# Performance work log

Measured on AMD Instinct MI355X. Metric: run time of the kernel, lower is better.

Reference implementation:

```python
import jax, jax.numpy as jnp
import numpy as np

N = 100000      # num_nodes
E = 1600000     # num_edges
F_IN = 5        # in_features
H = 64          # hidden_channels
HC = H // 2     # classifier hidden
L = 3           # num GCN layers
EPS = 1e-5      # BatchNorm eps


def setup_inputs() -> dict:
    key = jax.random.key(0)
    ks = jax.random.split(key, 12)
    s = 0.1
    return {
        "x": jax.random.normal(ks[0], (N, F_IN), dtype=jnp.float32),
        "edge_index": jax.random.randint(ks[1], (2, E), 0, N, dtype=jnp.int32),
        "W_in": jax.random.normal(ks[2], (F_IN, H), dtype=jnp.float32) * s,
        "b_in": jax.random.normal(ks[3], (H,), dtype=jnp.float32) * s,
        "conv_W": jax.random.normal(ks[4], (L, H, H), dtype=jnp.float32) * s,
        "conv_b": jax.random.normal(ks[5], (L, H), dtype=jnp.float32) * s,
        "bn_gamma": jnp.ones((L, H), dtype=jnp.float32),
        "bn_beta": jnp.zeros((L, H), dtype=jnp.float32),
        "W1": jax.random.normal(ks[6], (H, HC), dtype=jnp.float32) * s,
        "b1": jax.random.normal(ks[7], (HC,), dtype=jnp.float32) * s,
        "W2": jax.random.normal(ks[8], (HC, 1), dtype=jnp.float32) * s,
        "b2": jax.random.normal(ks[9], (1,), dtype=jnp.float32) * s,
    }


def reference(x, edge_index, W_in, b_in, conv_W, conv_b, bn_gamma, bn_beta, W1, b1, W2, b2):
    src, dst = edge_index[0], edge_index[1]

    # input projection + ReLU
    h = jax.nn.relu(x @ W_in + b_in)  # (N, H)

    # GCN symmetric normalization with self-loops (PyG GCNConv default):
    # deg includes the self-loop weight of 1.
    deg = jax.ops.segment_sum(jnp.ones((E,), dtype=h.dtype), dst, num_segments=N) + 1.0
    dinv = jax.lax.rsqrt(deg)                       # deg^{-1/2}, (N,)
    edge_coef = dinv[src] * dinv[dst]               # (E,)
    self_coef = dinv * dinv                         # (N,)

    for i in range(L):
        hw = h @ conv_W[i]                          # linear (no bias yet), (N, H)
        # gather -> scale -> scatter-add aggregation, plus self-loop term
        agg = jax.ops.segment_sum(hw[src] * edge_coef[:, None], dst, num_segments=N)
        agg = agg + hw * self_coef[:, None] + conv_b[i]
        # BatchNorm1d over nodes (batch statistics; eval dropout = identity)
        mean = jnp.mean(agg, axis=0)
        var = jnp.var(agg, axis=0)
        h = bn_gamma[i] * (agg - mean) * jax.lax.rsqrt(var + EPS) + bn_beta[i]
        h = jax.nn.relu(h)

    # classifier MLP: H -> H//2 -> 1, squeeze to (N,)
    logits = (jax.nn.relu(h @ W1 + b1) @ W2 + b2).squeeze(-1)
    return logits
```

## Files before the change

### kernel.cpp

```cpp
#include <hip/hip_runtime.h>

#define NN 100000
#define EE 1600000
#define EPSV 1e-5f
#define QW 12500

using short8 = __attribute__((ext_vector_type(8))) short;
using floatx4 = __attribute__((ext_vector_type(4))) float;

__device__ __forceinline__ unsigned short f2bf(float f) {
    union { float f; unsigned int u; } cv;
    cv.f = f;
    unsigned int u = cv.u;
    u += 0x7FFFu + ((u >> 16) & 1u);
    return (unsigned short)(u >> 16);
}

__device__ __forceinline__ float bf2f(unsigned short u) {
    union { unsigned int i; float f; } cv;
    cv.i = ((unsigned int)u) << 16;
    return cv.f;
}

__global__ void deg_kernel(const int* __restrict__ dst, int* __restrict__ degi8) {
    int e = blockIdx.x * 256 + threadIdx.x;
    if (e >= EE) return;
    int q = blockIdx.x & 7;
    atomicAdd(&degi8[q * NN + dst[e]], 1);
}

__global__ void scan1(const int* __restrict__ degi8, int* __restrict__ degi,
                      int* __restrict__ offsets, int* __restrict__ partial,
                      float* __restrict__ dinv) {
    __shared__ int sdata[256];
    int t = threadIdx.x;
    int n = blockIdx.x * 256 + t;
    int v = 0;
    if (n < NN) {
#pragma unroll
        for (int q = 0; q < 8; ++q) v += degi8[q * NN + n];
        degi[n] = v;
        dinv[n] = rsqrtf((float)v + 1.0f);
    }
    sdata[t] = v;
    __syncthreads();
    for (int off = 1; off < 256; off <<= 1) {
        int x = (t >= off) ? sdata[t - off] : 0;
        __syncthreads();
        sdata[t] += x;
        __syncthreads();
    }
    if (n < NN) offsets[n] = sdata[t] - v;
    if (t == 255) partial[blockIdx.x] = sdata[255];
}

__global__ void scan2(int* __restrict__ partial, int* __restrict__ partial_pref,
                      int nparts, float* __restrict__ stats) {
    __shared__ int sdata[512];
    int t = threadIdx.x;
    if (t < 384) stats[t] = 0.f;
    int v = (t < nparts) ? partial[t] : 0;
    sdata[t] = v;
    __syncthreads();
    for (int off = 1; off < 512; off <<= 1) {
        int x = (t >= off) ? sdata[t - off] : 0;
        __syncthreads();
        sdata[t] += x;
        __syncthreads();
    }
    if (t < nparts) partial_pref[t] = sdata[t] - v;
}

__global__ void fill_kernel(const int* __restrict__ src, const int* __restrict__ dst,
                            int* __restrict__ offsets,
                            const int* __restrict__ partial_pref,
                            const float* __restrict__ dinv,
                            int2* __restrict__ sorted) {
    int q = blockIdx.x & 7;
    int e = (blockIdx.x >> 3) * 256 + threadIdx.x;
    if (e >= EE) return;
    int d = dst[e];
    if ((unsigned)(d - q * QW) >= (unsigned)QW) return;
    int s = src[e];
    int idx = partial_pref[d >> 8] + atomicAdd(&offsets[d], 1);
    int2 rec;
    rec.x = s;
    rec.y = __float_as_int(dinv[s] * dinv[d]);
    sorted[idx] = rec;
}

__global__ __launch_bounds__(256) void gemm64_bn(const float* __restrict__ in,
                                                 const float* __restrict__ x,
                                                 const float* __restrict__ Win,
                                                 const float* __restrict__ bin,
                                                 const float* __restrict__ stats,
                                                 const float* __restrict__ gamma,
                                                 const float* __restrict__ beta,
                                                 const float* __restrict__ W,
                                                 unsigned short* __restrict__ out,
                                                 int mode) {
    __shared__ __align__(16) unsigned short As[64 * 72];
    __shared__ __align__(16) unsigned short Wt[64 * 72];
    __shared__ float scale[64], shift[64];
    __shared__ float Wins[320];
    __shared__ float bins[64];
    int t = threadIdx.x;
    if (mode == 1) {
        if (t < 64) {
            const float invN = 1.0f / (float)NN;
            float mean = stats[t] * invN;
            float var = stats[64 + t] * invN - mean * mean;
            float rstd = rsqrtf(var + EPSV);
            float sc = gamma[t] * rstd;
            scale[t] = sc;
            shift[t] = beta[t] - mean * sc;
        }
    } else {
        for (int i = t; i < 320; i += 256) Wins[i] = Win[i];
        if (t < 64) bins[t] = bin[t];
    }
    for (int i = t; i < 4096; i += 256) {
        int k = i >> 6, c = i & 63;
        Wt[c * 72 + k] = f2bf(W[k * 64 + c]);
    }
    __syncthreads();
    int base = blockIdx.x * 64;
    if (mode == 1) {
        for (int i = t; i < 4096; i += 256) {
            int r = i >> 6, c = i & 63;
            float v = 0.f;
            if (base + r < NN) {
                v = in[(base + r) * 64 + c];
                v = fmaxf(v * scale[c] + shift[c], 0.f);
            }
            As[r * 72 + c] = f2bf(v);
        }
    } else {
        for (int i = t; i < 4096; i += 256) {
            int r = i >> 6, c = i & 63;
            int n = base + r;
            float v = 0.f;
            if (n < NN) {
                float acc = bins[c];
#pragma unroll
                for (int k = 0; k < 5; ++k) acc += x[n * 5 + k] * Wins[k * 64 + c];
                v = fmaxf(acc, 0.f);
            }
            As[r * 72 + c] = f2bf(v);
        }
    }
    __syncthreads();
    int wv = t >> 6;
    int lane = t & 63;
    int quad = lane >> 4;
    int mm = lane & 15;
    short8 a0 = *(const short8*)&As[(wv * 16 + mm) * 72 + quad * 8];
    short8 a1 = *(const short8*)&As[(wv * 16 + mm) * 72 + 32 + quad * 8];
#pragma unroll
    for (int ct = 0; ct < 4; ++ct) {
        short8 b0 = *(const short8*)&Wt[(ct * 16 + mm) * 72 + quad * 8];
        short8 b1 = *(const short8*)&Wt[(ct * 16 + mm) * 72 + 32 + quad * 8];
        floatx4 acc = {0.f, 0.f, 0.f, 0.f};
        acc = __builtin_amdgcn_mfma_f32_16x16x32_bf16(a0, b0, acc, 0, 0, 0);
        acc = __builtin_amdgcn_mfma_f32_16x16x32_bf16(a1, b1, acc, 0, 0, 0);
#pragma unroll
        for (int reg = 0; reg < 4; ++reg) {
            int n = base + wv * 16 + quad * 4 + reg;
            if (n < NN) out[n * 64 + ct * 16 + mm] = f2bf(acc[reg]);
        }
    }
}

__global__ __launch_bounds__(256) void agg_kernel(const unsigned int* __restrict__ hw32,
                                                  const int2* __restrict__ sorted,
                                                  const int* __restrict__ offsets,
                                                  const int* __restrict__ partial_pref,
                                                  const int* __restrict__ degi,
                                                  const float* __restrict__ dinv,
                                                  const float* __restrict__ b,
                                                  float* __restrict__ agg,
                                                  float* __restrict__ stats) {
    int t = threadIdx.x;
    int lane = t & 63;
    int w = t >> 6;
    int half = lane >> 5;
    int c2 = lane & 31;
    float b0 = b[2 * c2], b1v = b[2 * c2 + 1];
    float bsx = 0.f, bsy = 0.f, bqx = 0.f, bqy = 0.f;
    for (int n = blockIdx.x * 4 + w; n < NN; n += gridDim.x * 4) {
        int cnt = degi[n];
        int start = partial_pref[n >> 8] + offsets[n] - cnt;
        float di = dinv[n];
        float ax = 0.f, ay = 0.f;
        if (half == 0) {
            unsigned int u = hw32[n * 32 + c2];
            float sc = di * di;
            ax = bf2f((unsigned short)(u & 0xffffu)) * sc + b0;
            ay = bf2f((unsigned short)(u >> 16)) * sc + b1v;
        }
        for (int base = 0; base < cnt; base += 64) {
            int m = min(64, cnt - base);
            int2 rec = make_int2(0, 0);
            if (lane < m) rec = sorted[start + base + lane];
            int k = 0;
            for (; k + 16 <= m; k += 16) {
                int e0 = k + half, e1 = k + 2 + half, e2 = k + 4 + half, e3 = k + 6 + half;
                int e4 = k + 8 + half, e5 = k + 10 + half, e6 = k + 12 + half, e7 = k + 14 + half;
                int s0 = __shfl(rec.x, e0), s1 = __shfl(rec.x, e1);
                int s2 = __shfl(rec.x, e2), s3 = __shfl(rec.x, e3);
                int s4 = __shfl(rec.x, e4), s5 = __shfl(rec.x, e5);
                int s6 = __shfl(rec.x, e6), s7 = __shfl(rec.x, e7);
                unsigned int u0 = hw32[s0 * 32 + c2];
                unsigned int u1 = hw32[s1 * 32 + c2];
                unsigned int u2 = hw32[s2 * 32 + c2];
                unsigned int u3 = hw32[s3 * 32 + c2];
                unsigned int u4 = hw32[s4 * 32 + c2];
                unsigned int u5 = hw32[s5 * 32 + c2];
                unsigned int u6 = hw32[s6 * 32 + c2];
                unsigned int u7 = hw32[s7 * 32 + c2];
                float c0 = __int_as_float(__shfl(rec.y, e0));
                float c1 = __int_as_float(__shfl(rec.y, e1));
                float c2f = __int_as_float(__shfl(rec.y, e2));
                float c3 = __int_as_float(__shfl(rec.y, e3));
                float c4 = __int_as_float(__shfl(rec.y, e4));
                float c5 = __int_as_float(__shfl(rec.y, e5));
                float c6 = __int_as_float(__shfl(rec.y, e6));
                float c7 = __int_as_float(__shfl(rec.y, e7));
                ax += bf2f((unsigned short)(u0 & 0xffffu)) * c0;
                ay += bf2f((unsigned short)(u0 >> 16)) * c0;
                ax += bf2f((unsigned short)(u1 & 0xffffu)) * c1;
                ay += bf2f((unsigned short)(u1 >> 16)) * c1;
                ax += bf2f((unsigned short)(u2 & 0xffffu)) * c2f;
                ay += bf2f((unsigned short)(u2 >> 16)) * c2f;
                ax += bf2f((unsigned short)(u3 & 0xffffu)) * c3;
                ay += bf2f((unsigned short)(u3 >> 16)) * c3;
                ax += bf2f((unsigned short)(u4 & 0xffffu)) * c4;
                ay += bf2f((unsigned short)(u4 >> 16)) * c4;
                ax += bf2f((unsigned short)(u5 & 0xffffu)) * c5;
                ay += bf2f((unsigned short)(u5 >> 16)) * c5;
                ax += bf2f((unsigned short)(u6 & 0xffffu)) * c6;
                ay += bf2f((unsigned short)(u6 >> 16)) * c6;
                ax += bf2f((unsigned short)(u7 & 0xffffu)) * c7;
                ay += bf2f((unsigned short)(u7 >> 16)) * c7;
            }
            for (; k + 4 <= m; k += 4) {
                int e0 = k + half, e1 = k + 2 + half;
                int s0 = __shfl(rec.x, e0), s1 = __shfl(rec.x, e1);
                unsigned int u0 = hw32[s0 * 32 + c2];
                unsigned int u1 = hw32[s1 * 32 + c2];
                float c0 = __int_as_float(__shfl(rec.y, e0));
                float c1 = __int_as_float(__shfl(rec.y, e1));
                ax += bf2f((unsigned short)(u0 & 0xffffu)) * c0;
                ay += bf2f((unsigned short)(u0 >> 16)) * c0;
                ax += bf2f((unsigned short)(u1 & 0xffffu)) * c1;
                ay += bf2f((unsigned short)(u1 >> 16)) * c1;
            }
            for (; k < m; k += 2) {
                int e = k + half;
                int s = __shfl(rec.x, e);
                float cf = __int_as_float(__shfl(rec.y, e));
                unsigned int u = hw32[s * 32 + c2];
                ax += bf2f((unsigned short)(u & 0xffffu)) * cf;
                ay += bf2f((unsigned short)(u >> 16)) * cf;
            }
        }
        ax += __shfl_xor(ax, 32);
        ay += __shfl_xor(ay, 32);
        if (half == 0) {
            float2 v = make_float2(ax, ay);
            *(float2*)&agg[n * 64 + 2 * c2] = v;
            bsx += ax;
            bsy += ay;
            bqx += ax * ax;
            bqy += ay * ay;
        }
    }
    __shared__ float red[2][4][64];
    if (half == 0) {
        red[0][w][2 * c2] = bsx;
        red[0][w][2 * c2 + 1] = bsy;
        red[1][w][2 * c2] = bqx;
        red[1][w][2 * c2 + 1] = bqy;
    }
    __syncthreads();
    if (w == 0) {
        int c = t;
        float s = red[0][0][c] + red[0][1][c] + red[0][2][c] + red[0][3][c];
        float ss = red[1][0][c] + red[1][1][c] + red[1][2][c] + red[1][3][c];
        atomicAdd(&stats[c], s);
        atomicAdd(&stats[64 + c], ss);
    }
}

__global__ __launch_bounds__(256) void classifier(const float* __restrict__ agg,
                                                  const float* __restrict__ stats,
                                                  const float* __restrict__ gamma,
                                                  const float* __restrict__ beta,
                                                  const float* __restrict__ W1,
                                                  const float* __restrict__ b1,
                                                  const float* __restrict__ W2,
                                                  const float* __restrict__ b2,
                                                  float* __restrict__ out) {
    __shared__ float W1s[2048];
    __shared__ float b1s[32];
    __shared__ float W2s[32];
    __shared__ float scale[64], shift[64];
    int t = threadIdx.x;
    for (int i = t; i < 2048; i += 256) W1s[i] = W1[i];
    if (t < 32) {
        b1s[t] = b1[t];
        W2s[t] = W2[t];
    }
    if (t < 64) {
        const float invN = 1.0f / (float)NN;
        float mean = stats[t] * invN;
        float var = stats[64 + t] * invN - mean * mean;
        float rstd = rsqrtf(var + EPSV);
        float sc = gamma[t] * rstd;
        scale[t] = sc;
        shift[t] = beta[t] - mean * sc;
    }
    __syncthreads();
    int n = blockIdx.x * 256 + t;
    if (n >= NN) return;
    float4 h4[16];
    const float4* hp = (const float4*)(agg + n * 64);
#pragma unroll
    for (int i = 0; i < 16; ++i) h4[i] = hp[i];
    float* hr = (float*)h4;
#pragma unroll
    for (int k = 0; k < 64; ++k) hr[k] = fmaxf(hr[k] * scale[k] + shift[k], 0.f);
    float o = b2[0];
    for (int c = 0; c < 32; ++c) {
        float z = b1s[c];
#pragma unroll
        for (int k = 0; k < 64; ++k) z += hr[k] * W1s[k * 32 + c];
        o += fmaxf(z, 0.f) * W2s[c];
    }
    out[n] = o;
}

extern "C" void kernel_launch(void* const* d_in, const int* in_sizes, int n_in,
                              void* d_out, int out_size, void* d_ws, size_t ws_size,
                              hipStream_t stream) {
    const float* x    = (const float*)d_in[0];
    const int*   ei   = (const int*)d_in[1];
    const float* Win  = (const float*)d_in[2];
    const float* bin  = (const float*)d_in[3];
    const float* cW   = (const float*)d_in[4];
    const float* cb   = (const float*)d_in[5];
    const float* gam  = (const float*)d_in[6];
    const float* bet  = (const float*)d_in[7];
    const float* W1   = (const float*)d_in[8];
    const float* b1   = (const float*)d_in[9];
    const float* W2   = (const float*)d_in[10];
    const float* b2   = (const float*)d_in[11];
    float* out = (float*)d_out;

    unsigned short* hw = (unsigned short*)d_ws;
    float* agg   = (float*)d_ws + NN * 32;
    float* dinv  = agg + NN * 64;
    float* stats = dinv + NN;
    int*  degi        = (int*)(stats + 3 * 128);
    int*  offsets     = degi + NN;
    int2* sorted      = (int2*)(offsets + NN);
    int*  partial     = (int*)(sorted + EE);
    int*  partial_pref = partial + 512;
    int*  degi8       = partial_pref + 512;

    const int* src = ei;
    const int* dst = ei + EE;

    const int NB = (NN + 255) / 256;
    const int EB = (EE + 255) / 256;

    (void)hipMemsetAsync(degi8, 0, 8 * NN * sizeof(int), stream);

    deg_kernel<<<EB, 256, 0, stream>>>(dst, degi8);
    scan1<<<NB, 256, 0, stream>>>(degi8, degi, offsets, partial, dinv);
    scan2<<<1, 512, 0, stream>>>(partial, partial_pref, NB, stats);
    fill_kernel<<<EB * 8, 256, 0, stream>>>(src, dst, offsets, partial_pref, dinv, sorted);

    for (int i = 0; i < 3; ++i) {
        gemm64_bn<<<(NN + 63) / 64, 256, 0, stream>>>(
            agg, x, Win, bin, stats + (i - 1) * 128, gam + (i - 1) * 64,
            bet + (i - 1) * 64, cW + i * 4096, hw, i > 0 ? 1 : 0);
        agg_kernel<<<2048, 256, 0, stream>>>((const unsigned int*)hw, sorted, offsets,
                                             partial_pref, degi, dinv, cb + i * 64, agg,
                                             stats + i * 128);
    }

    classifier<<<(NN + 255) / 256, 256, 0, stream>>>(agg, stats + 2 * 128, gam + 2 * 64,
                                                     bet + 2 * 64, W1, b1, W2, b2, out);
}
```

Before: 524.9 us.

## Split hw into column-group planes and aggregate per-group for cache locality

The GEMM output is stored as four column-group planes of 16 bf16 features per node instead of a row-major 64-wide layout. The aggregation kernel assigns each block one column group and one half of the nodes, so each block gathers 32-byte rows from a smaller plane that fits better in cache. Eight lanes cover a row and eight edges are processed in parallel, with nontemporal loads and stores for the streaming edge and output data. The edge lists are now re-read once per column group (four times overall), and the loop hardcodes a grid of 2048 blocks. If the launch configuration is not updated to match, coverage will be incorrect.

```diff
diff --git a/kernel.cpp b/kernel.cpp
--- a/kernel.cpp
+++ b/kernel.cpp
@@ -4,6 +4,7 @@
 #define EE 1600000
 #define EPSV 1e-5f
 #define QW 12500
+#define HN 50000
 
 using short8 = __attribute__((ext_vector_type(8))) short;
 using floatx4 = __attribute__((ext_vector_type(4))) float;
@@ -166,7 +167,7 @@
 #pragma unroll
         for (int reg = 0; reg < 4; ++reg) {
             int n = base + wv * 16 + quad * 4 + reg;
-            if (n < NN) out[n * 64 + ct * 16 + mm] = f2bf(acc[reg]);
+            if (n < NN) out[(ct * NN + n) * 16 + mm] = f2bf(acc[reg]);
         }
     }
 }
@@ -183,112 +184,73 @@
     int t = threadIdx.x;
     int lane = t & 63;
     int w = t >> 6;
-    int half = lane >> 5;
-    int c2 = lane & 31;
-    float b0 = b[2 * c2], b1v = b[2 * c2 + 1];
+    int q = blockIdx.x & 7;
+    int g = q & 3;
+    int h = q >> 2;
+    int bi = blockIdx.x >> 3;
+    int cwu = lane & 7;
+    int eg = lane >> 3;
+    int gbase = g * NN;
+    float b0 = b[g * 16 + 2 * cwu], b1v = b[g * 16 + 2 * cwu + 1];
     float bsx = 0.f, bsy = 0.f, bqx = 0.f, bqy = 0.f;
-    for (int n = blockIdx.x * 4 + w; n < NN; n += gridDim.x * 4) {
+    int n0 = h * HN;
+    for (int n = n0 + bi * 4 + w; n < n0 + HN; n += 256 * 4) {
         int cnt = degi[n];
         int start = partial_pref[n >> 8] + offsets[n] - cnt;
-        float di = dinv[n];
         float ax = 0.f, ay = 0.f;
-        if (half == 0) {
-            unsigned int u = hw32[n * 32 + c2];
+        if (eg == 0) {
+            unsigned int u = hw32[(unsigned)(gbase + n) * 8 + cwu];
+            float di = dinv[n];
             float sc = di * di;
             ax = bf2f((unsigned short)(u & 0xffffu)) * sc + b0;
             ay = bf2f((unsigned short)(u >> 16)) * sc + b1v;
         }
-        for (int base = 0; base < cnt; base += 64) {
-            int m = min(64, cnt - base);
-            int2 rec = make_int2(0, 0);
-            if (lane < m) rec = sorted[start + base + lane];
-            int k = 0;
-            for (; k + 16 <= m; k += 16) {
-                int e0 = k + half, e1 = k + 2 + half, e2 = k + 4 + half, e3 = k + 6 + half;
-                int e4 = k + 8 + half, e5 = k + 10 + half, e6 = k + 12 + half, e7 = k + 14 + half;
-                int s0 = __shfl(rec.x, e0), s1 = __shfl(rec.x, e1);
-                int s2 = __shfl(rec.x, e2), s3 = __shfl(rec.x, e3);
-                int s4 = __shfl(rec.x, e4), s5 = __shfl(rec.x, e5);
-                int s6 = __shfl(rec.x, e6), s7 = __shfl(rec.x, e7);
-                unsigned int u0 = hw32[s0 * 32 + c2];
-                unsigned int u1 = hw32[s1 * 32 + c2];
-                unsigned int u2 = hw32[s2 * 32 + c2];
-                unsigned int u3 = hw32[s3 * 32 + c2];
-                unsigned int u4 = hw32[s4 * 32 + c2];
-                unsigned int u5 = hw32[s5 * 32 + c2];
-                unsigned int u6 = hw32[s6 * 32 + c2];
-                unsigned int u7 = hw32[s7 * 32 + c2];
-                float c0 = __int_as_float(__shfl(rec.y, e0));
-                float c1 = __int_as_float(__shfl(rec.y, e1));
-                float c2f = __int_as_float(__shfl(rec.y, e2));
-                float c3 = __int_as_float(__shfl(rec.y, e3));
-                float c4 = __int_as_float(__shfl(rec.y, e4));
-                float c5 = __int_as_float(__shfl(rec.y, e5));
-                float c6 = __int_as_float(__shfl(rec.y, e6));
-                float c7 = __int_as_float(__shfl(rec.y, e7));
-                ax += bf2f((unsigned short)(u0 & 0xffffu)) * c0;
-                ay += bf2f((unsigned short)(u0 >> 16)) * c0;
-                ax += bf2f((unsigned short)(u1 & 0xffffu)) * c1;
-                ay += bf2f((unsigned short)(u1 >> 16)) * c1;
-                ax += bf2f((unsigned short)(u2 & 0xffffu)) * c2f;
-                ay += bf2f((unsigned short)(u2 >> 16)) * c2f;
-                ax += bf2f((unsigned short)(u3 & 0xffffu)) * c3;
-                ay += bf2f((unsigned short)(u3 >> 16)) * c3;
-                ax += bf2f((unsigned short)(u4 & 0xffffu)) * c4;
-                ay += bf2f((unsigned short)(u4 >> 16)) * c4;
-                ax += bf2f((unsigned short)(u5 & 0xffffu)) * c5;
-                ay += bf2f((unsigned short)(u5 >> 16)) * c5;
-                ax += bf2f((unsigned short)(u6 & 0xffffu)) * c6;
-                ay += bf2f((unsigned short)(u6 >> 16)) * c6;
-                ax += bf2f((unsigned short)(u7 & 0xffffu)) * c7;
-                ay += bf2f((unsigned short)(u7 >> 16)) * c7;
-            }
-            for (; k + 4 <= m; k += 4) {
-                int e0 = k + half, e1 = k + 2 + half;
-                int s0 = __shfl(rec.x, e0), s1 = __shfl(rec.x, e1);
-                unsigned int u0 = hw32[s0 * 32 + c2];
-                unsigned int u1 = hw32[s1 * 32 + c2];
-                float c0 = __int_as_float(__shfl(rec.y, e0));
-                float c1 = __int_as_float(__shfl(rec.y, e1));
-                ax += bf2f((unsigned short)(u0 & 0xffffu)) * c0;
-                ay += bf2f((unsigned short)(u0 >> 16)) * c0;
-                ax += bf2f((unsigned short)(u1 & 0xffffu)) * c1;
-                ay += bf2f((unsigned short)(u1 >> 16)) * c1;
-            }
-            for (; k < m; k += 2) {
-                int e = k + half;
-                int s = __shfl(rec.x, e);
-                float cf = __int_as_float(__shfl(rec.y, e));
-                unsigned int u = hw32[s * 32 + c2];
-                ax += bf2f((unsigned short)(u & 0xffffu)) * cf;
-                ay += bf2f((unsigned short)(u >> 16)) * cf;
-            }
-        }
+        for (int base = 0; base < cnt; base += 16) {
+            int e0 = base + eg, e1 = base + 8 + eg;
+            long long rr0 = 0, rr1 = 0;
+            if (e0 < cnt) rr0 = __builtin_nontemporal_load((const long long*)&sorted[start + e0]);
+            if (e1 < cnt) rr1 = __builtin_nontemporal_load((const long long*)&sorted[start + e1]);
+            int s0 = (int)(unsigned int)(rr0 & 0xffffffffLL);
+            int s1 = (int)(unsigned int)(rr1 & 0xffffffffLL);
+            unsigned int u0 = hw32[(unsigned)(gbase + s0) * 8 + cwu];
+            unsigned int u1 = hw32[(unsigned)(gbase + s1) * 8 + cwu];
+            float c0 = __int_as_float((int)(rr0 >> 32));
+            float c1 = __int_as_float((int)(rr1 >> 32));
+            ax += bf2f((unsigned short)(u0 & 0xffffu)) * c0;
+            ay += bf2f((unsigned short)(u0 >> 16)) * c0;
+            ax += bf2f((unsigned short)(u1 & 0xffffu)) * c1;
+            ay += bf2f((unsigned short)(u1 >> 16)) * c1;
+        }
+        ax += __shfl_xor(ax, 8);
+        ay += __shfl_xor(ay, 8);
+        ax += __shfl_xor(ax, 16);
+        ay += __shfl_xor(ay, 16);
         ax += __shfl_xor(ax, 32);
         ay += __shfl_xor(ay, 32);
-        if (half == 0) {
-            float2 v = make_float2(ax, ay);
-            *(float2*)&agg[n * 64 + 2 * c2] = v;
+        if (eg == 0) {
+            unsigned long long pv =
+                ((unsigned long long)__float_as_uint(ay) << 32) | __float_as_uint(ax);
+            __builtin_nontemporal_store(pv,
+                (unsigned long long*)&agg[n * 64 + g * 16 + 2 * cwu]);
             bsx += ax;
             bsy += ay;
             bqx += ax * ax;
             bqy += ay * ay;
         }
     }
-    __shared__ float red[2][4][64];
-    if (half == 0) {
-        red[0][w][2 * c2] = bsx;
-        red[0][w][2 * c2 + 1] = bsy;
-        red[1][w][2 * c2] = bqx;
-        red[1][w][2 * c2 + 1] = bqy;
-    }
-    __syncthreads();
-    if (w == 0) {
-        int c = t;
-        float s = red[0][0][c] + red[0][1][c] + red[0][2][c] + red[0][3][c];
-        float ss = red[1][0][c] + red[1][1][c] + red[1][2][c] + red[1][3][c];
-        atomicAdd(&stats[c], s);
-        atomicAdd(&stats[64 + c], ss);
+    __shared__ float red[2][4][16];
+    if (eg == 0) {
+        red[0][w][2 * cwu] = bsx;
+        red[0][w][2 * cwu + 1] = bsy;
+        red[1][w][2 * cwu] = bqx;
+        red[1][w][2 * cwu + 1] = bqy;
+    }
+    __syncthreads();
+    if (w == 0 && lane < 16) {
+        float s = red[0][0][lane] + red[0][1][lane] + red[0][2][lane] + red[0][3][lane];
+        float ss = red[1][0][lane] + red[1][1][lane] + red[1][2][lane] + red[1][3][lane];
+        atomicAdd(&stats[g * 16 + lane], s);
+        atomicAdd(&stats[64 + g * 16 + lane], ss);
     }
 }
 
```

Result: slower. 634.9 us (+21.0%).

## Widen aggregation gathers to 8-byte loads and drop dst-partitioned fill passes

Applied to the files above, without the earlier changes.

The aggregation kernel now has each lane load four bf16 features (uint2) instead of two, so one wavefront covers four edges at a time using 16 lanes per edge. A two-stage xor-shuffle reduction combines the partial sums and the result is stored as float4. Separately, the CSR fill kernel no longer runs eight quarter-range passes that each rescan every edge; it does a single pass. That cuts the redundant edge reads but gives up the destination-range locality the eight passes provided for the atomics and the scattered writes.

```diff
diff --git a/kernel.cpp b/kernel.cpp
--- a/kernel.cpp
+++ b/kernel.cpp
@@ -3,7 +3,6 @@
 #define NN 100000
 #define EE 1600000
 #define EPSV 1e-5f
-#define QW 12500
 
 using short8 = __attribute__((ext_vector_type(8))) short;
 using floatx4 = __attribute__((ext_vector_type(4))) float;
@@ -76,11 +75,9 @@
                             const int* __restrict__ partial_pref,
                             const float* __restrict__ dinv,
                             int2* __restrict__ sorted) {
-    int q = blockIdx.x & 7;
-    int e = (blockIdx.x >> 3) * 256 + threadIdx.x;
+    int e = blockIdx.x * 256 + threadIdx.x;
     if (e >= EE) return;
     int d = dst[e];
-    if ((unsigned)(d - q * QW) >= (unsigned)QW) return;
     int s = src[e];
     int idx = partial_pref[d >> 8] + atomicAdd(&offsets[d], 1);
     int2 rec;
@@ -171,7 +168,7 @@
     }
 }
 
-__global__ __launch_bounds__(256) void agg_kernel(const unsigned int* __restrict__ hw32,
+__global__ __launch_bounds__(256) void agg_kernel(const uint2* __restrict__ hw64,
                                                   const int2* __restrict__ sorted,
                                                   const int* __restrict__ offsets,
                                                   const int* __restrict__ partial_pref,
@@ -183,20 +180,23 @@
     int t = threadIdx.x;
     int lane = t & 63;
     int w = t >> 6;
-    int half = lane >> 5;
-    int c2 = lane & 31;
-    float b0 = b[2 * c2], b1v = b[2 * c2 + 1];
-    float bsx = 0.f, bsy = 0.f, bqx = 0.f, bqy = 0.f;
+    int eg = lane >> 4;
+    int cu = lane & 15;
+    float b0 = b[4 * cu], b1v = b[4 * cu + 1], b2v = b[4 * cu + 2], b3v = b[4 * cu + 3];
+    float bs0 = 0.f, bs1 = 0.f, bs2 = 0.f, bs3 = 0.f;
+    float bq0 = 0.f, bq1 = 0.f, bq2 = 0.f, bq3 = 0.f;
     for (int n = blockIdx.x * 4 + w; n < NN; n += gridDim.x * 4) {
         int cnt = degi[n];
         int start = partial_pref[n >> 8] + offsets[n] - cnt;
-        float di = dinv[n];
-        float ax = 0.f, ay = 0.f;
-        if (half == 0) {
-            unsigned int u = hw32[n * 32 + c2];
+        float a0 = 0.f, a1 = 0.f, a2 = 0.f, a3 = 0.f;
+        if (eg == 0) {
+            uint2 u = hw64[(unsigned)n * 16 + cu];
+            float di = dinv[n];
             float sc = di * di;
-            ax = bf2f((unsigned short)(u & 0xffffu)) * sc + b0;
-            ay = bf2f((unsigned short)(u >> 16)) * sc + b1v;
+            a0 = bf2f((unsigned short)(u.x & 0xffffu)) * sc + b0;
+            a1 = bf2f((unsigned short)(u.x >> 16)) * sc + b1v;
+            a2 = bf2f((unsigned short)(u.y & 0xffffu)) * sc + b2v;
+            a3 = bf2f((unsigned short)(u.y >> 16)) * sc + b3v;
         }
         for (int base = 0; base < cnt; base += 64) {
             int m = min(64, cnt - base);
@@ -204,83 +204,80 @@
             if (lane < m) rec = sorted[start + base + lane];
             int k = 0;
             for (; k + 16 <= m; k += 16) {
-                int e0 = k + half, e1 = k + 2 + half, e2 = k + 4 + half, e3 = k + 6 + half;
-                int e4 = k + 8 + half, e5 = k + 10 + half, e6 = k + 12 + half, e7 = k + 14 + half;
+                int e0 = k + eg, e1 = k + 4 + eg, e2 = k + 8 + eg, e3 = k + 12 + eg;
                 int s0 = __shfl(rec.x, e0), s1 = __shfl(rec.x, e1);
                 int s2 = __shfl(rec.x, e2), s3 = __shfl(rec.x, e3);
-                int s4 = __shfl(rec.x, e4), s5 = __shfl(rec.x, e5);
-                int s6 = __shfl(rec.x, e6), s7 = __shfl(rec.x, e7);
-                unsigned int u0 = hw32[s0 * 32 + c2];
-                unsigned int u1 = hw32[s1 * 32 + c2];
-                unsigned int u2 = hw32[s2 * 32 + c2];
-                unsigned int u3 = hw32[s3 * 32 + c2];
-                unsigned int u4 = hw32[s4 * 32 + c2];
-                unsigned int u5 = hw32[s5 * 32 + c2];
-                unsigned int u6 = hw32[s6 * 32 + c2];
-                unsigned int u7 = hw32[s7 * 32 + c2];
+                uint2 u0 = hw64[(unsigned)s0 * 16 + cu];
+                uint2 u1 = hw64[(unsigned)s1 * 16 + cu];
+                uint2 u2 = hw64[(unsigned)s2 * 16 + cu];
+                uint2 u3 = hw64[(unsigned)s3 * 16 + cu];
                 float c0 = __int_as_float(__shfl(rec.y, e0));
                 float c1 = __int_as_float(__shfl(rec.y, e1));
-                float c2f = __int_as_float(__shfl(rec.y, e2));
+                float c2 = __int_as_float(__shfl(rec.y, e2));
                 float c3 = __int_as_float(__shfl(rec.y, e3));
-                float c4 = __int_as_float(__shfl(rec.y, e4));
-                float c5 = __int_as_float(__shfl(rec.y, e5));
-                float c6 = __int_as_float(__shfl(rec.y, e6));
-                float c7 = __int_as_float(__shfl(rec.y, e7));
-                ax += bf2f((unsigned short)(u0 & 0xffffu)) * c0;
-                ay += bf2f((unsigned short)(u0 >> 16)) * c0;
-                ax += bf2f((unsigned short)(u1 & 0xffffu)) * c1;
-                ay += bf2f((unsigned short)(u1 >> 16)) * c1;
-                ax += bf2f((unsigned short)(u2 & 0xffffu)) * c2f;
-                ay += bf2f((unsigned short)(u2 >> 16)) * c2f;
-                ax += bf2f((unsigned short)(u3 & 0xffffu)) * c3;
-                ay += bf2f((unsigned short)(u3 >> 16)) * c3;
-                ax += bf2f((unsigned short)(u4 & 0xffffu)) * c4;
-                ay += bf2f((unsigned short)(u4 >> 16)) * c4;
-                ax += bf2f((unsigned short)(u5 & 0xffffu)) * c5;
-                ay += bf2f((unsigned short)(u5 >> 16)) * c5;
-                ax += bf2f((unsigned short)(u6 & 0xffffu)) * c6;
-                ay += bf2f((unsigned short)(u6 >> 16)) * c6;
-                ax += bf2f((unsigned short)(u7 & 0xffffu)) * c7;
-                ay += bf2f((unsigned short)(u7 >> 16)) * c7;
+                a0 += bf2f((unsigned short)(u0.x & 0xffffu)) * c0;
+                a1 += bf2f((unsigned short)(u0.x >> 16)) * c0;
+                a2 += bf2f((unsigned short)(u0.y & 0xffffu)) * c0;
+                a3 += bf2f((unsigned short)(u0.y >> 16)) * c0;
+                a0 += bf2f((unsigned short)(u1.x & 0xffffu)) * c1;
+                a1 += bf2f((unsigned short)(u1.x >> 16)) * c1;
+                a2 += bf2f((unsigned short)(u1.y & 0xffffu)) * c1;
+                a3 += bf2f((unsigned short)(u1.y >> 16)) * c1;
+                a0 += bf2f((unsigned short)(u2.x & 0xffffu)) * c2;
+                a1 += bf2f((unsigned short)(u2.x >> 16)) * c2;
+                a2 += bf2f((unsigned short)(u2.y & 0xffffu)) * c2;
+                a3 += bf2f((unsigned short)(u2.y >> 16)) * c2;
+                a0 += bf2f((unsigned short)(u3.x & 0xffffu)) * c3;
+                a1 += bf2f((unsigned short)(u3.x >> 16)) * c3;
+                a2 += bf2f((unsigned short)(u3.y & 0xffffu)) * c3;
+                a3 += bf2f((unsigned short)(u3.y >> 16)) * c3;
             }
             for (; k + 4 <= m; k += 4) {
-                int e0 = k + half, e1 = k + 2 + half;
-                int s0 = __shfl(rec.x, e0), s1 = __shfl(rec.x, e1);
-                unsigned int u0 = hw32[s0 * 32 + c2];
-                unsigned int u1 = hw32[s1 * 32 + c2];
-                float c0 = __int_as_float(__shfl(rec.y, e0));
-                float c1 = __int_as_float(__shfl(rec.y, e1));
-                ax += bf2f((unsigned short)(u0 & 0xffffu)) * c0;
-                ay += bf2f((unsigned short)(u0 >> 16)) * c0;
-                ax += bf2f((unsigned short)(u1 & 0xffffu)) * c1;
-                ay += bf2f((unsigned short)(u1 >> 16)) * c1;
-            }
-            for (; k < m; k += 2) {
-                int e = k + half;
+                int e = k + eg;
                 int s = __shfl(rec.x, e);
-                float cf = __int_as_float(__shfl(rec.y, e));
-                unsigned int u = hw32[s * 32 + c2];
-                ax += bf2f((unsigned short)(u & 0xffffu)) * cf;
-                ay += bf2f((unsigned short)(u >> 16)) * cf;
-            }
-        }
-        ax += __shfl_xor(ax, 32);
-        ay += __shfl_xor(ay, 32);
-        if (half == 0) {
-            float2 v = make_float2(ax, ay);
-            *(float2*)&agg[n * 64 + 2 * c2] = v;
-            bsx += ax;
-            bsy += ay;
-            bqx += ax * ax;
-            bqy += ay * ay;
+                uint2 u = hw64[(unsigned)s * 16 + cu];
+                float c = __int_as_float(__shfl(rec.y, e));
+                a0 += bf2f((unsigned short)(u.x & 0xffffu)) * c;
+                a1 += bf2f((unsigned short)(u.x >> 16)) * c;
+                a2 += bf2f((unsigned short)(u.y & 0xffffu)) * c;
+                a3 += bf2f((unsigned short)(u.y >> 16)) * c;
+            }
+            if (k < m) {
+                int e = k + eg;
+                int s = __shfl(rec.x, e);
+                uint2 u = hw64[(unsigned)s * 16 + cu];
+                float c = __int_as_float(__shfl(rec.y, e));
+                a0 += bf2f((unsigned short)(u.x & 0xffffu)) * c;
+                a1 += bf2f((unsigned short)(u.x >> 16)) * c;
+                a2 += bf2f((unsigned short)(u.y & 0xffffu)) * c;
+                a3 += bf2f((unsigned short)(u.y >> 16)) * c;
+            }
+        }
+        a0 += __shfl_xor(a0, 16);
+        a1 += __shfl_xor(a1, 16);
+        a2 += __shfl_xor(a2, 16);
+        a3 += __shfl_xor(a3, 16);
+        a0 += __shfl_xor(a0, 32);
+        a1 += __shfl_xor(a1, 32);
+        a2 += __shfl_xor(a2, 32);
+        a3 += __shfl_xor(a3, 32);
+        if (eg == 0) {
+            float4 v = make_float4(a0, a1, a2, a3);
+            *(float4*)&agg[(unsigned)n * 64 + 4 * cu] = v;
+            bs0 += a0; bs1 += a1; bs2 += a2; bs3 += a3;
+            bq0 += a0 * a0; bq1 += a1 * a1; bq2 += a2 * a2; bq3 += a3 * a3;
         }
     }
     __shared__ float red[2][4][64];
-    if (half == 0) {
-        red[0][w][2 * c2] = bsx;
-        red[0][w][2 * c2 + 1] = bsy;
-        red[1][w][2 * c2] = bqx;
-        red[1][w][2 * c2 + 1] = bqy;
+    if (eg == 0) {
+        red[0][w][4 * cu] = bs0;
+        red[0][w][4 * cu + 1] = bs1;
+        red[0][w][4 * cu + 2] = bs2;
+        red[0][w][4 * cu + 3] = bs3;
+        red[1][w][4 * cu] = bq0;
+        red[1][w][4 * cu + 1] = bq1;
+        red[1][w][4 * cu + 2] = bq2;
+        red[1][w][4 * cu + 3] = bq3;
     }
     __syncthreads();
     if (w == 0) {
@@ -379,13 +376,13 @@
     deg_kernel<<<EB, 256, 0, stream>>>(dst, degi8);
     scan1<<<NB, 256, 0, stream>>>(degi8, degi, offsets, partial, dinv);
     scan2<<<1, 512, 0, stream>>>(partial, partial_pref, NB, stats);
-    fill_kernel<<<EB * 8, 256, 0, stream>>>(src, dst, offsets, partial_pref, dinv, sorted);
+    fill_kernel<<<EB, 256, 0, stream>>>(src, dst, offsets, partial_pref, dinv, sorted);
 
     for (int i = 0; i < 3; ++i) {
         gemm64_bn<<<(NN + 63) / 64, 256, 0, stream>>>(
             agg, x, Win, bin, stats + (i - 1) * 128, gam + (i - 1) * 64,
             bet + (i - 1) * 64, cW + i * 4096, hw, i > 0 ? 1 : 0);
-        agg_kernel<<<2048, 256, 0, stream>>>((const unsigned int*)hw, sorted, offsets,
+        agg_kernel<<<2048, 256, 0, stream>>>((const uint2*)hw, sorted, offsets,
                                              partial_pref, degi, dinv, cb + i * 64, agg,
                                              stats + i * 128);
     }
```

Result: no change. 524.9 us (+0.0%).
